# Kernel optimization log

Measured on AMD Instinct MI355X. Metric: run time of the kernel, lower is better.

## Reference

```python
import jax, jax.numpy as jnp
import numpy as np

N, E, IN, OUT = 50000, 800000, 128, 128
R = 5  # num_rels + 1 (last slice is the self-loop weight)


def setup_inputs() -> dict:
    key = jax.random.key(0)
    k = jax.random.split(key, 6)
    x = jax.random.normal(k[0], (N, IN), jnp.float32)
    src = jax.random.randint(k[1], (E,), 0, N)
    dst = jax.random.randint(k[2], (E,), 0, N)
    rel = jax.random.randint(k[3], (E,), 0, R - 1)  # edge rel_type in [0, num_rels)
    xavier = np.sqrt(2.0) * np.sqrt(6.0 / (IN + OUT))  # gain('relu') * xavier bound scale
    weight = jax.random.uniform(k[4], (R, IN, OUT), jnp.float32, -xavier, xavier)
    bias = jax.random.uniform(k[5], (R, OUT), jnp.float32, -xavier, xavier)
    return dict(x=x, weight=weight, bias=bias, src=src, dst=dst, rel=rel)


def reference(x, weight, bias, src, dst, rel):
    num_nodes = x.shape[0]
    num_edge_rels = weight.shape[0] - 1
    x_src = x[src]  # [E, IN] per-edge source gather
    # Per-edge message: x_src @ weight[rel] + bias[rel].
    # Grouped-GEMM style: one dense GEMM per relation, select by mask
    # (avoids materializing [E, IN, OUT] per-edge weights).
    msg = jnp.zeros((src.shape[0], weight.shape[2]), x.dtype)
    for r in range(num_edge_rels):
        hr = x_src @ weight[r] + bias[r]  # [E, OUT]
        msg = jnp.where((rel == r)[:, None], hr, msg)
    # Max-aggregation onto destination nodes; DGL fills 0 for nodes w/o in-edges.
    agg = jax.ops.segment_max(msg, dst, num_segments=num_nodes)  # [N, OUT]
    deg = jax.ops.segment_sum(jnp.ones_like(dst, jnp.float32), dst, num_segments=num_nodes)
    agg = jnp.where((deg > 0)[:, None], agg, jnp.zeros((), x.dtype))
    # Self-loop transform with last weight/bias slice.
    h = x @ weight[-1] + bias[-1] + agg
    return h
```

## Files before the change

### kernel.cpp

```cpp
#include <hip/hip_runtime.h>

#define NNODES 50000
#define NEDGES 800000
#define DIM    128
#define NRELS  4
#define NBLK2  25
#define NDB    1280
#define ILV    (2*NDB)
#define NFB    3125
#define EPB    12500
#define NHC    64
#define RNG    25000

typedef __attribute__((ext_vector_type(8))) short bf16x8;
typedef __attribute__((ext_vector_type(8))) unsigned short u16x8;
typedef __attribute__((ext_vector_type(4))) float f32x4;

#define SSRC_OFF 0
#define CNT_OFF  3200000
#define BSUM_OFF 3404800
#define RANK_OFF 3405056
#define PCNT_OFF 5005056
#define WT_OFF   11405056
#define XBF_OFF  11568896
#define H_OFF    24368896

__device__ __forceinline__ unsigned short f2bf(float f) {
  unsigned u = __float_as_uint(f);
  return (unsigned short)((u + 0x7FFFu + ((u >> 16) & 1u)) >> 16);
}

__global__ void k_prep(const float* __restrict__ x, unsigned short* __restrict__ xbf,
                       const float* __restrict__ W, unsigned short* __restrict__ Wt) {
  int i = blockIdx.x * blockDim.x + threadIdx.x;
  if (i < NNODES * DIM / 8) {
    const float4* p = (const float4*)x + i * 2;
    float4 v0 = p[0], v1 = p[1];
    u16x8 o;
    o[0] = f2bf(v0.x); o[1] = f2bf(v0.y); o[2] = f2bf(v0.z); o[3] = f2bf(v0.w);
    o[4] = f2bf(v1.x); o[5] = f2bf(v1.y); o[6] = f2bf(v1.z); o[7] = f2bf(v1.w);
    *(u16x8*)(xbf + i * 8) = o;
  }
  if (i < 5 * DIM * DIM) {
    int r = i >> 14, rem = i & 16383, k = rem >> 7, c = rem & 127;
    Wt[(r << 14) + (c << 7) + k] = f2bf(W[i]);
  }
}

__global__ __launch_bounds__(1024) void k_hist(const int* __restrict__ dst,
                                               unsigned short* __restrict__ rank,
                                               unsigned short* __restrict__ pcnt) {
  __shared__ unsigned lh[RNG / 2];
  int c = blockIdx.x >> 1;
  int r0 = (blockIdx.x & 1) * RNG;
  for (int i = threadIdx.x; i < RNG / 2; i += 1024) lh[i] = 0u;
  __syncthreads();
  int e0 = c * EPB;
  for (int e = e0 + threadIdx.x; e < e0 + EPB; e += 1024) {
    int d = dst[e] - r0;
    if ((unsigned)d < (unsigned)RNG) {
      unsigned old = atomicAdd(&lh[d >> 1], (d & 1) ? 65536u : 1u);
      rank[e] = (unsigned short)((old >> ((d & 1) << 4)) & 0xFFFFu);
    }
  }
  __syncthreads();
  unsigned* prow = (unsigned*)(pcnt + (size_t)c * NNODES + r0);
  for (int i = threadIdx.x; i < RNG / 2; i += 1024) prow[i] = lh[i];
}

__global__ void k_scanB(unsigned short* __restrict__ pcnt, unsigned* __restrict__ cnt,
                        unsigned* __restrict__ bsum) {
  __shared__ unsigned sh[256];
  int tid = threadIdx.x;
  int bin0 = blockIdx.x * 2048 + tid * 8;
  unsigned run[8] = {0, 0, 0, 0, 0, 0, 0, 0};
  if (bin0 < NNODES) {
    for (int b = 0; b < NHC; b++) {
      size_t off = (size_t)b * NNODES + bin0;
      u16x8 v = *(const u16x8*)(pcnt + off);
      u16x8 w;
#pragma unroll
      for (int j = 0; j < 8; j++) { w[j] = (unsigned short)run[j]; run[j] += v[j]; }
      *(u16x8*)(pcnt + off) = w;
    }
  }
  unsigned tsum = 0;
#pragma unroll
  for (int j = 0; j < 8; j++) tsum += run[j];
  sh[tid] = tsum;
  __syncthreads();
  for (int off = 1; off < 256; off <<= 1) {
    unsigned t = (tid >= off) ? sh[tid - off] : 0u;
    __syncthreads();
    sh[tid] += t;
    __syncthreads();
  }
  unsigned r = sh[tid] - tsum;
#pragma unroll
  for (int j = 0; j < 8; j++) { unsigned t = run[j]; cnt[bin0 + j] = r; r += t; }
  if (tid == 255) bsum[blockIdx.x] = sh[255];
}

__global__ void k_fix(unsigned* __restrict__ cnt, const unsigned* __restrict__ bsum) {
  int blk = blockIdx.x;
  if (blk == 0) return;
  unsigned p = 0;
  for (int k = 0; k < blk; k++) p += bsum[k];
  int base = blk * 2048 + threadIdx.x * 8;
#pragma unroll
  for (int j = 0; j < 8; j++) cnt[base + j] += p;
}

__global__ __launch_bounds__(256, 2) void k_dfill(
    const unsigned short* __restrict__ xbf, const unsigned short* __restrict__ Wt,
    const float* __restrict__ bias, unsigned short* __restrict__ H,
    float* __restrict__ out, const int* __restrict__ rel, const int* __restrict__ dst,
    const int* __restrict__ src, const unsigned* __restrict__ cnt,
    const unsigned short* __restrict__ rank, const unsigned short* __restrict__ pfx,
    unsigned* __restrict__ ssrc) {
  int b = blockIdx.x;
  if (b >= ILV || (b & 1)) {
    int fi = (b < ILV) ? (b >> 1) : (b - NDB);
    int e = fi * 256 + threadIdx.x;
    if (e < NEDGES) {
      int r = rel[e]; r = r < 0 ? 0 : (r > NRELS - 1 ? NRELS - 1 : r);
      int d = dst[e];
      unsigned pos = cnt[d] + (unsigned)pfx[(size_t)(e / EPB) * NNODES + d] + (unsigned)rank[e];
      ssrc[pos] = (unsigned)(r * NNODES + src[e]);
    }
    return;
  }
  __shared__ unsigned short st[4][2048];
  int di = b >> 1;
  int lane = threadIdx.x & 63;
  int wv = threadIdx.x >> 6;
  int r = di % 5;
  int tl = di / 5;
  const int NT = NNODES / 16;
  int col = lane & 15, quad = lane >> 4;

  const unsigned short* wr = Wt + (r << 14);
  bf16x8 B[8][4];
  float bs[8];
#pragma unroll
  for (int ct = 0; ct < 8; ct++) {
#pragma unroll
    for (int kk = 0; kk < 4; kk++)
      B[ct][kk] = *(const bf16x8*)(wr + ((ct * 16 + col) << 7) + kk * 32 + quad * 8);
    bs[ct] = bias[(r << 7) + ct * 16 + col];
  }

  for (int t = tl * 4 + wv; t < NT; t += 1024) {
    int n0 = t * 16;
    int na = n0 + col;
    bf16x8 a0 = *(const bf16x8*)(xbf + (na << 7) + quad * 8);
    bf16x8 a1 = *(const bf16x8*)(xbf + (na << 7) + 32 + quad * 8);
    bf16x8 a2 = *(const bf16x8*)(xbf + (na << 7) + 64 + quad * 8);
    bf16x8 a3 = *(const bf16x8*)(xbf + (na << 7) + 96 + quad * 8);

    if (r < NRELS) {
#pragma unroll
      for (int ct = 0; ct < 8; ct++) {
        f32x4 acc = {0.f, 0.f, 0.f, 0.f};
        acc = __builtin_amdgcn_mfma_f32_16x16x32_bf16(a0, B[ct][0], acc, 0, 0, 0);
        acc = __builtin_amdgcn_mfma_f32_16x16x32_bf16(a1, B[ct][1], acc, 0, 0, 0);
        acc = __builtin_amdgcn_mfma_f32_16x16x32_bf16(a2, B[ct][2], acc, 0, 0, 0);
        acc = __builtin_amdgcn_mfma_f32_16x16x32_bf16(a3, B[ct][3], acc, 0, 0, 0);
        int cc = ct * 16 + col;
#pragma unroll
        for (int j = 0; j < 4; j++) st[wv][(quad * 4 + j) * 128 + cc] = f2bf(acc[j] + bs[ct]);
      }
      unsigned short* gb = H + (((size_t)(r * NNODES + n0)) << 7);
#pragma unroll
      for (int s = 0; s < 4; s++) {
        int off = s * 512 + lane * 8;
        *(u16x8*)(gb + off) = *(const u16x8*)(&st[wv][off]);
      }
    } else {
#pragma unroll
      for (int ct = 0; ct < 8; ct++) {
        f32x4 acc = {0.f, 0.f, 0.f, 0.f};
        acc = __builtin_amdgcn_mfma_f32_16x16x32_bf16(a0, B[ct][0], acc, 0, 0, 0);
        acc = __builtin_amdgcn_mfma_f32_16x16x32_bf16(a1, B[ct][1], acc, 0, 0, 0);
        acc = __builtin_amdgcn_mfma_f32_16x16x32_bf16(a2, B[ct][2], acc, 0, 0, 0);
        acc = __builtin_amdgcn_mfma_f32_16x16x32_bf16(a3, B[ct][3], acc, 0, 0, 0);
        int cc = ct * 16 + col;
#pragma unroll
        for (int j = 0; j < 4; j++)
          out[((size_t)(n0 + quad * 4 + j) << 7) + (unsigned)cc] = acc[j] + bs[ct];
      }
    }
  }
}

__global__ __launch_bounds__(256, 4) void k_agg(
    const unsigned* __restrict__ cnt, const unsigned* __restrict__ ssrc,
    const uint4* __restrict__ H4, float* __restrict__ out) {
  int lane = threadIdx.x & 15;
  int q = threadIdx.x >> 4;
  int n = blockIdx.x * 16 + q;
  unsigned base = cnt[n];
  int deg = (int)(cnt[n + 1] - base);

  float m0 = -3.0e38f, m1 = -3.0e38f, m2 = -3.0e38f, m3 = -3.0e38f;
  float m4 = -3.0e38f, m5 = -3.0e38f, m6 = -3.0e38f, m7 = -3.0e38f;
#define UNP(v)                                        \
  m0 = fmaxf(m0, __uint_as_float((v).x << 16));       \
  m1 = fmaxf(m1, __uint_as_float((v).x & 0xFFFF0000u)); \
  m2 = fmaxf(m2, __uint_as_float((v).y << 16));       \
  m3 = fmaxf(m3, __uint_as_float((v).y & 0xFFFF0000u)); \
  m4 = fmaxf(m4, __uint_as_float((v).z << 16));       \
  m5 = fmaxf(m5, __uint_as_float((v).z & 0xFFFF0000u)); \
  m6 = fmaxf(m6, __uint_as_float((v).w << 16));       \
  m7 = fmaxf(m7, __uint_as_float((v).w & 0xFFFF0000u))
  int i = 0;
  for (; i + 4 <= deg; i += 4) {
    unsigned c0 = ssrc[base + i], c1 = ssrc[base + i + 1];
    unsigned c2 = ssrc[base + i + 2], c3 = ssrc[base + i + 3];
    uint4 v0 = H4[((size_t)c0 << 4) + lane];
    uint4 v1 = H4[((size_t)c1 << 4) + lane];
    uint4 v2 = H4[((size_t)c2 << 4) + lane];
    uint4 v3 = H4[((size_t)c3 << 4) + lane];
    UNP(v0); UNP(v1); UNP(v2); UNP(v3);
  }
  for (; i < deg; i++) {
    unsigned c = ssrc[base + i];
    uint4 v = H4[((size_t)c << 4) + lane];
    UNP(v);
  }
#undef UNP
  float4* op = (float4*)(out + ((size_t)n << 7)) + lane * 2;
  float4 s0 = op[0], s1 = op[1];
  if (deg > 0) {
    s0.x += m0; s0.y += m1; s0.z += m2; s0.w += m3;
    s1.x += m4; s1.y += m5; s1.z += m6; s1.w += m7;
  }
  op[0] = s0; op[1] = s1;
}

extern "C" void kernel_launch(void* const* d_in, const int* in_sizes, int n_in,
                              void* d_out, int out_size, void* d_ws, size_t ws_size,
                              hipStream_t stream) {
  const float* x = (const float*)d_in[0];
  const float* W = (const float*)d_in[1];
  const float* bias = (const float*)d_in[2];
  const int* src = (const int*)d_in[3];
  const int* dst = (const int*)d_in[4];
  const int* rel = (const int*)d_in[5];

  char* ws = (char*)d_ws;
  unsigned* ssrc = (unsigned*)(ws + SSRC_OFF);
  unsigned* cnt = (unsigned*)(ws + CNT_OFF);
  unsigned* bsum = (unsigned*)(ws + BSUM_OFF);
  unsigned short* rank = (unsigned short*)(ws + RANK_OFF);
  unsigned short* pcnt = (unsigned short*)(ws + PCNT_OFF);
  unsigned short* Wt = (unsigned short*)(ws + WT_OFF);
  unsigned short* xbf = (unsigned short*)(ws + XBF_OFF);
  unsigned short* H = (unsigned short*)(ws + H_OFF);
  float* out = (float*)d_out;

  hipLaunchKernelGGL(k_prep, dim3(3125), dim3(256), 0, stream, x, xbf, W, Wt);
  hipLaunchKernelGGL(k_hist, dim3(NHC * 2), dim3(1024), 0, stream, dst, rank, pcnt);
  hipLaunchKernelGGL(k_scanB, dim3(NBLK2), dim3(256), 0, stream, pcnt, cnt, bsum);
  hipLaunchKernelGGL(k_fix, dim3(NBLK2), dim3(256), 0, stream, cnt, bsum);
  hipLaunchKernelGGL(k_dfill, dim3(NDB + NFB), dim3(256), 0, stream, xbf, Wt, bias, H, out, rel,
                     dst, src, cnt, rank, pcnt, ssrc);
  hipLaunchKernelGGL(k_agg, dim3(3125), dim3(256), 0, stream, cnt, ssrc, (const uint4*)H, out);
}
```

Measured before the change: 215.0 us.

## Fuse prep and histogram kernels, reshape dense grid, widen aggregation gather

Merges the bf16 conversion kernel and the destination histogram kernel into one launch, with the first blocks doing histograms and the rest doing conversion at 1024 threads per block. The dense GEMM part of k_dfill drops from 1280 interleaved blocks to 640 blocks grouped by relation, and the edge-scatter blocks are no longer interleaved with them. H and output stores become nontemporal. The aggregation loop now issues 8 gathers per iteration, clamping indices so there is no scalar tail. The aim is fewer launches and more memory-level parallelism, at the cost of redundant loads for low-degree nodes and less dense-phase parallelism.

```diff
diff --git a/kernel.cpp b/kernel.cpp
--- a/kernel.cpp
+++ b/kernel.cpp
@@ -5,12 +5,13 @@
 #define DIM    128
 #define NRELS  4
 #define NBLK2  25
-#define NDB    1280
-#define ILV    (2*NDB)
+#define DBLK   128
+#define NDB    (5*DBLK)
 #define NFB    3125
 #define EPB    12500
 #define NHC    64
 #define RNG    25000
+#define NPB    782
 
 typedef __attribute__((ext_vector_type(8))) short bf16x8;
 typedef __attribute__((ext_vector_type(8))) unsigned short u16x8;
@@ -30,9 +31,31 @@
   return (unsigned short)((u + 0x7FFFu + ((u >> 16) & 1u)) >> 16);
 }
 
-__global__ void k_prep(const float* __restrict__ x, unsigned short* __restrict__ xbf,
-                       const float* __restrict__ W, unsigned short* __restrict__ Wt) {
-  int i = blockIdx.x * blockDim.x + threadIdx.x;
+__global__ __launch_bounds__(1024) void k_ph(
+    const float* __restrict__ x, unsigned short* __restrict__ xbf,
+    const float* __restrict__ W, unsigned short* __restrict__ Wt,
+    const int* __restrict__ dst, unsigned short* __restrict__ rank,
+    unsigned short* __restrict__ pcnt) {
+  __shared__ unsigned lh[RNG / 2];
+  if (blockIdx.x < NHC * 2) {
+    int c = blockIdx.x >> 1;
+    int r0 = (blockIdx.x & 1) * RNG;
+    for (int i = threadIdx.x; i < RNG / 2; i += 1024) lh[i] = 0u;
+    __syncthreads();
+    int e0 = c * EPB;
+    for (int e = e0 + threadIdx.x; e < e0 + EPB; e += 1024) {
+      int d = dst[e] - r0;
+      if ((unsigned)d < (unsigned)RNG) {
+        unsigned old = atomicAdd(&lh[d >> 1], (d & 1) ? 65536u : 1u);
+        rank[e] = (unsigned short)((old >> ((d & 1) << 4)) & 0xFFFFu);
+      }
+    }
+    __syncthreads();
+    unsigned* prow = (unsigned*)(pcnt + (size_t)c * NNODES + r0);
+    for (int i = threadIdx.x; i < RNG / 2; i += 1024) prow[i] = lh[i];
+    return;
+  }
+  int i = (blockIdx.x - NHC * 2) * 1024 + threadIdx.x;
   if (i < NNODES * DIM / 8) {
     const float4* p = (const float4*)x + i * 2;
     float4 v0 = p[0], v1 = p[1];
@@ -45,27 +68,6 @@
     int r = i >> 14, rem = i & 16383, k = rem >> 7, c = rem & 127;
     Wt[(r << 14) + (c << 7) + k] = f2bf(W[i]);
   }
-}
-
-__global__ __launch_bounds__(1024) void k_hist(const int* __restrict__ dst,
-                                               unsigned short* __restrict__ rank,
-                                               unsigned short* __restrict__ pcnt) {
-  __shared__ unsigned lh[RNG / 2];
-  int c = blockIdx.x >> 1;
-  int r0 = (blockIdx.x & 1) * RNG;
-  for (int i = threadIdx.x; i < RNG / 2; i += 1024) lh[i] = 0u;
-  __syncthreads();
-  int e0 = c * EPB;
-  for (int e = e0 + threadIdx.x; e < e0 + EPB; e += 1024) {
-    int d = dst[e] - r0;
-    if ((unsigned)d < (unsigned)RNG) {
-      unsigned old = atomicAdd(&lh[d >> 1], (d & 1) ? 65536u : 1u);
-      rank[e] = (unsigned short)((old >> ((d & 1) << 4)) & 0xFFFFu);
-    }
-  }
-  __syncthreads();
-  unsigned* prow = (unsigned*)(pcnt + (size_t)c * NNODES + r0);
-  for (int i = threadIdx.x; i < RNG / 2; i += 1024) prow[i] = lh[i];
 }
 
 __global__ void k_scanB(unsigned short* __restrict__ pcnt, unsigned* __restrict__ cnt,
@@ -118,10 +120,8 @@
     const int* __restrict__ src, const unsigned* __restrict__ cnt,
     const unsigned short* __restrict__ rank, const unsigned short* __restrict__ pfx,
     unsigned* __restrict__ ssrc) {
-  int b = blockIdx.x;
-  if (b >= ILV || (b & 1)) {
-    int fi = (b < ILV) ? (b >> 1) : (b - NDB);
-    int e = fi * 256 + threadIdx.x;
+  if (blockIdx.x >= NDB) {
+    int e = (blockIdx.x - NDB) * 256 + threadIdx.x;
     if (e < NEDGES) {
       int r = rel[e]; r = r < 0 ? 0 : (r > NRELS - 1 ? NRELS - 1 : r);
       int d = dst[e];
@@ -131,11 +131,9 @@
     return;
   }
   __shared__ unsigned short st[4][2048];
-  int di = b >> 1;
   int lane = threadIdx.x & 63;
   int wv = threadIdx.x >> 6;
-  int r = di % 5;
-  int tl = di / 5;
+  int r = blockIdx.x / DBLK;
   const int NT = NNODES / 16;
   int col = lane & 15, quad = lane >> 4;
 
@@ -150,7 +148,7 @@
     bs[ct] = bias[(r << 7) + ct * 16 + col];
   }
 
-  for (int t = tl * 4 + wv; t < NT; t += 1024) {
+  for (int t = (blockIdx.x % DBLK) * 4 + wv; t < NT; t += DBLK * 4) {
     int n0 = t * 16;
     int na = n0 + col;
     bf16x8 a0 = *(const bf16x8*)(xbf + (na << 7) + quad * 8);
@@ -174,7 +172,7 @@
 #pragma unroll
       for (int s = 0; s < 4; s++) {
         int off = s * 512 + lane * 8;
-        *(u16x8*)(gb + off) = *(const u16x8*)(&st[wv][off]);
+        __builtin_nontemporal_store(*(const u16x8*)(&st[wv][off]), (u16x8*)(gb + off));
       }
     } else {
 #pragma unroll
@@ -187,7 +185,8 @@
         int cc = ct * 16 + col;
 #pragma unroll
         for (int j = 0; j < 4; j++)
-          out[((size_t)(n0 + quad * 4 + j) << 7) + (unsigned)cc] = acc[j] + bs[ct];
+          __builtin_nontemporal_store(acc[j] + bs[ct],
+                                      out + ((size_t)(n0 + quad * 4 + j) << 7) + (unsigned)cc);
       }
     }
   }
@@ -204,29 +203,37 @@
 
   float m0 = -3.0e38f, m1 = -3.0e38f, m2 = -3.0e38f, m3 = -3.0e38f;
   float m4 = -3.0e38f, m5 = -3.0e38f, m6 = -3.0e38f, m7 = -3.0e38f;
-#define UNP(v)                                        \
-  m0 = fmaxf(m0, __uint_as_float((v).x << 16));       \
+#define UNP(v)                                          \
+  m0 = fmaxf(m0, __uint_as_float((v).x << 16));         \
   m1 = fmaxf(m1, __uint_as_float((v).x & 0xFFFF0000u)); \
-  m2 = fmaxf(m2, __uint_as_float((v).y << 16));       \
+  m2 = fmaxf(m2, __uint_as_float((v).y << 16));         \
   m3 = fmaxf(m3, __uint_as_float((v).y & 0xFFFF0000u)); \
-  m4 = fmaxf(m4, __uint_as_float((v).z << 16));       \
+  m4 = fmaxf(m4, __uint_as_float((v).z << 16));         \
   m5 = fmaxf(m5, __uint_as_float((v).z & 0xFFFF0000u)); \
-  m6 = fmaxf(m6, __uint_as_float((v).w << 16));       \
+  m6 = fmaxf(m6, __uint_as_float((v).w << 16));         \
   m7 = fmaxf(m7, __uint_as_float((v).w & 0xFFFF0000u))
-  int i = 0;
-  for (; i + 4 <= deg; i += 4) {
-    unsigned c0 = ssrc[base + i], c1 = ssrc[base + i + 1];
-    unsigned c2 = ssrc[base + i + 2], c3 = ssrc[base + i + 3];
-    uint4 v0 = H4[((size_t)c0 << 4) + lane];
-    uint4 v1 = H4[((size_t)c1 << 4) + lane];
-    uint4 v2 = H4[((size_t)c2 << 4) + lane];
-    uint4 v3 = H4[((size_t)c3 << 4) + lane];
-    UNP(v0); UNP(v1); UNP(v2); UNP(v3);
-  }
-  for (; i < deg; i++) {
-    unsigned c = ssrc[base + i];
-    uint4 v = H4[((size_t)c << 4) + lane];
-    UNP(v);
+  if (deg > 0) {
+    int lim = deg - 1;
+    for (int i = 0; i < deg; i += 8) {
+      unsigned c0 = ssrc[base + min(i, lim)];
+      unsigned c1 = ssrc[base + min(i + 1, lim)];
+      unsigned c2 = ssrc[base + min(i + 2, lim)];
+      unsigned c3 = ssrc[base + min(i + 3, lim)];
+      unsigned c4 = ssrc[base + min(i + 4, lim)];
+      unsigned c5 = ssrc[base + min(i + 5, lim)];
+      unsigned c6 = ssrc[base + min(i + 6, lim)];
+      unsigned c7 = ssrc[base + min(i + 7, lim)];
+      uint4 v0 = H4[((size_t)c0 << 4) + lane];
+      uint4 v1 = H4[((size_t)c1 << 4) + lane];
+      uint4 v2 = H4[((size_t)c2 << 4) + lane];
+      uint4 v3 = H4[((size_t)c3 << 4) + lane];
+      uint4 v4 = H4[((size_t)c4 << 4) + lane];
+      uint4 v5 = H4[((size_t)c5 << 4) + lane];
+      uint4 v6 = H4[((size_t)c6 << 4) + lane];
+      uint4 v7 = H4[((size_t)c7 << 4) + lane];
+      UNP(v0); UNP(v1); UNP(v2); UNP(v3);
+      UNP(v4); UNP(v5); UNP(v6); UNP(v7);
+    }
   }
 #undef UNP
   float4* op = (float4*)(out + ((size_t)n << 7)) + lane * 2;
@@ -259,8 +266,8 @@
   unsigned short* H = (unsigned short*)(ws + H_OFF);
   float* out = (float*)d_out;
 
-  hipLaunchKernelGGL(k_prep, dim3(3125), dim3(256), 0, stream, x, xbf, W, Wt);
-  hipLaunchKernelGGL(k_hist, dim3(NHC * 2), dim3(1024), 0, stream, dst, rank, pcnt);
+  hipLaunchKernelGGL(k_ph, dim3(NHC * 2 + NPB), dim3(1024), 0, stream, x, xbf, W, Wt, dst, rank,
+                     pcnt);
   hipLaunchKernelGGL(k_scanB, dim3(NBLK2), dim3(256), 0, stream, pcnt, cnt, bsum);
   hipLaunchKernelGGL(k_fix, dim3(NBLK2), dim3(256), 0, stream, cnt, bsum);
   hipLaunchKernelGGL(k_dfill, dim3(NDB + NFB), dim3(256), 0, stream, xbf, Wt, bias, H, out, rel,
```

New measurement: 180.1 us. 16.2% less time.
